# Kernel optimization log

Measured on AMD Instinct MI355X. Metric: run time of the kernel, lower is better.

## Reference

```python
import jax, jax.numpy as jnp
import numpy as np

N_NODES = 50000
N_EDGES = 300000
D = 256  # node/edge feature dim; MLP input = 3*D = 768


def setup_inputs() -> dict:
    key = jax.random.key(0)
    ks = jax.random.split(key, 5)
    x_node = jax.random.normal(ks[0], (N_NODES, D), dtype=jnp.float32)
    x_edge = jax.random.normal(ks[1], (N_EDGES, D), dtype=jnp.float32)
    edge_index = jax.random.randint(ks[2], (2, N_EDGES), 0, N_NODES, dtype=jnp.int64)
    # MLP params: Linear(3*D, D) -> ReLU -> Linear(D, D)
    W1 = jax.random.normal(ks[3], (3 * D, D), dtype=jnp.float32) * (1.0 / np.sqrt(3 * D))
    b1 = jnp.zeros((D,), dtype=jnp.float32)
    W2 = jax.random.normal(ks[4], (D, D), dtype=jnp.float32) * (1.0 / np.sqrt(D))
    b2 = jnp.zeros((D,), dtype=jnp.float32)
    return {"x_node": x_node, "x_edge": x_edge, "edge_index": edge_index,
            "W1": W1, "b1": b1, "W2": W2, "b2": b2}


def reference(x_node, x_edge, edge_index, W1, b1, W2, b2):
    # gather src/dst node feats and concat with edge feats: [E, 3*D]
    src = x_node[edge_index[0]]
    dst = x_node[edge_index[1]]
    h = jnp.concatenate([src, dst, x_edge], axis=1)
    # MLP (custom_func): Linear -> ReLU -> Linear
    h = jax.nn.relu(h @ W1 + b1)
    x_edge_ = h @ W2 + b2
    return x_edge_
```

## Files before the change

### kernel.cpp

```cpp
#include <hip/hip_runtime.h>


typedef __attribute__((ext_vector_type(8))) short short8;
typedef __attribute__((ext_vector_type(4))) float f32x4;

typedef __attribute__((address_space(1))) unsigned int* gp1_t;
typedef __attribute__((address_space(3))) unsigned int* lp3_t;

#define AS_OFF 0
#define BS_OFF 16384
#define HS_OFF 49152
#define SMEM_SZ 114688
#define LDO 260

__device__ __forceinline__ unsigned short f2b(float f) {
  unsigned int u = __float_as_uint(f);
  return (unsigned short)((u + 0x7FFFu + ((u >> 16) & 1u)) >> 16);
}
__device__ __forceinline__ unsigned int f2b2(float lo, float hi) {
  return (unsigned int)f2b(lo) | ((unsigned int)f2b(hi) << 16);
}
__device__ __forceinline__ void gload16(const void* g, void* l) {
  __builtin_amdgcn_global_load_lds((gp1_t)g, (lp3_t)l, 16, 0, 0);
}

__global__ void prep_w_kernel(const float* __restrict__ w,
                              unsigned short* __restrict__ wp, int total) {
  int i = blockIdx.x * 256 + threadIdx.x;
  if (i >= total) return;
  int kc = i >> 13;
  int rem = i & 8191;
  int n = rem >> 5;
  int kin = rem & 31;
  wp[i] = f2b(w[(size_t)(kc * 32 + kin) * 256 + n]);
}

__global__ void conv_bf16_kernel(const float* __restrict__ x,
                                 unsigned short* __restrict__ y, int n4) {
  int i = blockIdx.x * 256 + threadIdx.x;
  if (i >= n4) return;
  float4 v = ((const float4*)x)[i];
  ushort4 u;
  u.x = f2b(v.x); u.y = f2b(v.y); u.z = f2b(v.z); u.w = f2b(v.w);
  ((ushort4*)y)[i] = u;
}

__global__ __launch_bounds__(512, 2) void edge_mlp_kernel(
    const float* __restrict__ xnode, const float* __restrict__ xedge,
    const int* __restrict__ eidx,
    const unsigned short* __restrict__ nodeb, int use_nodeb,
    const unsigned short* __restrict__ wt1p, const float* __restrict__ b1,
    const unsigned short* __restrict__ wt2p, const float* __restrict__ b2,
    float* __restrict__ out, int E) {
  __shared__ __align__(16) char smem[SMEM_SZ];
  char* As = smem + AS_OFF;
  char* Bs = smem + BS_OFF;
  char* Hs = smem + HS_OFF;

  const int t = threadIdx.x;
  const int w = t >> 6, l = t & 63;
  const int lr = l & 15, lk = l >> 4;
  const int wr = w >> 2, wc = w & 3;
  const int row4 = t >> 2;
  const int c4 = t & 3;

  const int ebase = blockIdx.x * 128;
  int e = ebase + row4;
  if (e >= E) e = E - 1;
  const int isrc = eidx[e], idst = eidx[E + e];

  f32x4 acc[4][4];
#pragma unroll
  for (int i = 0; i < 4; ++i)
#pragma unroll
    for (int j = 0; j < 4; ++j) acc[i][j] = (f32x4)0.0f;

  auto stageB = [&](const unsigned short* wp, int kc, int buf) {
    const char* g = (const char*)wp + (size_t)kc * 16384 + t * 16;
    char* lb = Bs + buf * 16384 + (w << 10);
    gload16(g, lb);
    gload16(g + 8192, lb + 8192);
  };
  auto stageA_node = [&](int kc, int buf) {
    const int node = (kc < 8) ? isrc : idst;
    const char* g = (const char*)nodeb + (size_t)node * 512 + (kc & 7) * 64 + c4 * 16;
    gload16(g, As + buf * 8192 + (w << 10));
  };
  auto stageA_load = [&](int kc, float4& m0, float4& m1) {
    const float* src;
    if (kc < 8)        src = xnode + (size_t)isrc * 256 + kc * 32 + c4 * 8;
    else if (kc < 16)  src = xnode + (size_t)idst * 256 + (kc - 8) * 32 + c4 * 8;
    else               src = xedge + (size_t)e * 256 + (kc - 16) * 32 + c4 * 8;
    m0 = *(const float4*)src;
    m1 = *(const float4*)(src + 4);
  };
  auto stageA_write = [&](int buf, float4 m0, float4 m1) {
    uint4 u;
    u.x = f2b2(m0.x, m0.y); u.y = f2b2(m0.z, m0.w);
    u.z = f2b2(m1.x, m1.y); u.w = f2b2(m1.z, m1.w);
    *(uint4*)(As + buf * 8192 + t * 16) = u;
  };

  auto compute1 = [&](int buf) {
    short8 af[4], bf[4];
    const char* ab = As + buf * 8192;
    const char* bb = Bs + buf * 16384;
#pragma unroll
    for (int mi = 0; mi < 4; ++mi)
      af[mi] = *(const short8*)(ab + (wr * 64 + mi * 16 + lr) * 64 + lk * 16);
#pragma unroll
    for (int ni = 0; ni < 4; ++ni)
      bf[ni] = *(const short8*)(bb + (wc * 64 + ni * 16 + lr) * 64 + lk * 16);
#pragma unroll
    for (int mi = 0; mi < 4; ++mi)
#pragma unroll
      for (int ni = 0; ni < 4; ++ni)
        acc[mi][ni] = __builtin_amdgcn_mfma_f32_16x16x32_bf16(
            af[mi], bf[ni], acc[mi][ni], 0, 0, 0);
  };

  stageB(wt1p, 0, 0);
  if (use_nodeb) {
    stageA_node(0, 0);
  } else {
    float4 a0, a1;
    stageA_load(0, a0, a1);
    stageA_write(0, a0, a1);
  }
  __syncthreads();

  for (int kc = 0; kc < 24; ++kc) {
    const int cur = kc & 1, nb = cur ^ 1;
    float4 m0, m1;
    bool man = false;
    if (kc < 23) {
      const int nk = kc + 1;
      stageB(wt1p, nk, nb);
      if (use_nodeb && nk < 16) {
        stageA_node(nk, nb);
      } else {
        stageA_load(nk, m0, m1);
        man = true;
      }
    } else {
      stageB(wt2p, 0, nb);
    }
    compute1(cur);
    if (man) stageA_write(nb, m0, m1);
    __syncthreads();
  }

#pragma unroll
  for (int ni = 0; ni < 4; ++ni) {
    const int col = wc * 64 + ni * 16 + lr;
    const float bias = b1[col];
    const int chunk = col >> 3;
    const int cb = (col & 7) * 2;
#pragma unroll
    for (int mi = 0; mi < 4; ++mi)
#pragma unroll
      for (int r = 0; r < 4; ++r) {
        const int row = wr * 64 + mi * 16 + lk * 4 + r;
        float v = acc[mi][ni][r] + bias;
        v = v > 0.f ? v : 0.f;
        *(unsigned short*)(Hs + row * 512 + ((chunk ^ (row & 7)) * 16) + cb) = f2b(v);
        acc[mi][ni][r] = 0.f;
      }
  }
  __syncthreads();

  for (int kc2 = 0; kc2 < 8; ++kc2) {
    const int cur = kc2 & 1, nb = cur ^ 1;
    if (kc2 < 7) stageB(wt2p, kc2 + 1, nb);
    {
      short8 af[4], bf[4];
      const char* bb = Bs + cur * 16384;
#pragma unroll
      for (int mi = 0; mi < 4; ++mi) {
        const int row = wr * 64 + mi * 16 + lr;
        af[mi] = *(const short8*)(Hs + row * 512 + (((kc2 * 4 + lk) ^ (row & 7)) * 16));
      }
#pragma unroll
      for (int ni = 0; ni < 4; ++ni)
        bf[ni] = *(const short8*)(bb + (wc * 64 + ni * 16 + lr) * 64 + lk * 16);
#pragma unroll
      for (int mi = 0; mi < 4; ++mi)
#pragma unroll
        for (int ni = 0; ni < 4; ++ni)
          acc[mi][ni] = __builtin_amdgcn_mfma_f32_16x16x32_bf16(
              af[mi], bf[ni], acc[mi][ni], 0, 0, 0);
    }
    __syncthreads();
  }

  float* outst = (float*)smem;
#pragma unroll
  for (int p = 0; p < 2; ++p) {
    __syncthreads();
    if (wr == p) {
#pragma unroll
      for (int ni = 0; ni < 4; ++ni) {
        const int col = wc * 64 + ni * 16 + lr;
        const float bias = b2[col];
#pragma unroll
        for (int mi = 0; mi < 4; ++mi)
#pragma unroll
          for (int r = 0; r < 4; ++r)
            outst[(mi * 16 + lk * 4 + r) * LDO + col] = acc[mi][ni][r] + bias;
      }
    }
    __syncthreads();
#pragma unroll
    for (int it = 0; it < 8; ++it) {
      const int idx = it * 2048 + t * 4;
      const int lrow = idx >> 8;
      const int cc = idx & 255;
      const int grow = ebase + p * 64 + lrow;
      if (grow < E)
        *(float4*)(out + (size_t)grow * 256 + cc) =
            *(const float4*)(outst + lrow * LDO + cc);
    }
  }
}

extern "C" void kernel_launch(void* const* d_in, const int* in_sizes, int n_in,
                              void* d_out, int out_size, void* d_ws, size_t ws_size,
                              hipStream_t stream) {
  const float* xnode = (const float*)d_in[0];
  const float* xedge = (const float*)d_in[1];
  const int* eidx = (const int*)d_in[2];
  const float* W1 = (const float*)d_in[3];
  const float* b1 = (const float*)d_in[4];
  const float* W2 = (const float*)d_in[5];
  const float* b2 = (const float*)d_in[6];
  float* out = (float*)d_out;

  const int NN = in_sizes[0] / 256;
  const int E = in_sizes[1] / 256;

  char* ws = (char*)d_ws;
  unsigned short* wt1p = (unsigned short*)ws;
  unsigned short* wt2p = (unsigned short*)(ws + 24 * 16384);
  unsigned short* nodeb = (unsigned short*)(ws + 32 * 16384);
  const size_t need = (size_t)32 * 16384 + (size_t)NN * 512;
  const int use_nodeb = (ws_size >= need) ? 1 : 0;

  prep_w_kernel<<<(24 * 8192 + 255) / 256, 256, 0, stream>>>(W1, wt1p, 24 * 8192);
  prep_w_kernel<<<(8 * 8192 + 255) / 256, 256, 0, stream>>>(W2, wt2p, 8 * 8192);
  if (use_nodeb) {
    const int n4 = NN * 64;
    conv_bf16_kernel<<<(n4 + 255) / 256, 256, 0, stream>>>(xnode, nodeb, n4);
  }

  edge_mlp_kernel<<<(E + 127) / 128, 512, 0, stream>>>(
      xnode, xedge, eidx, nodeb, use_nodeb, wt1p, b1, wt2p, b2, out, E);
}
```

Before: 332.2 us.

## Shrink edge MLP tile to 64 edges with 4 waves and pack H writes

```diff
diff --git a/kernel.cpp b/kernel.cpp
--- a/kernel.cpp
+++ b/kernel.cpp
@@ -8,9 +8,9 @@
 typedef __attribute__((address_space(3))) unsigned int* lp3_t;
 
 #define AS_OFF 0
-#define BS_OFF 16384
-#define HS_OFF 49152
-#define SMEM_SZ 114688
+#define BS_OFF 8192
+#define HS_OFF 40960
+#define SMEM_SZ 73728
 #define LDO 260
 
 __device__ __forceinline__ unsigned short f2b(float f) {
@@ -45,7 +45,7 @@
   ((ushort4*)y)[i] = u;
 }
 
-__global__ __launch_bounds__(512, 2) void edge_mlp_kernel(
+__global__ __launch_bounds__(256, 2) void edge_mlp_kernel(
     const float* __restrict__ xnode, const float* __restrict__ xedge,
     const int* __restrict__ eidx,
     const unsigned short* __restrict__ nodeb, int use_nodeb,
@@ -60,11 +60,10 @@
   const int t = threadIdx.x;
   const int w = t >> 6, l = t & 63;
   const int lr = l & 15, lk = l >> 4;
-  const int wr = w >> 2, wc = w & 3;
   const int row4 = t >> 2;
   const int c4 = t & 3;
 
-  const int ebase = blockIdx.x * 128;
+  const int ebase = blockIdx.x * 64;
   int e = ebase + row4;
   if (e >= E) e = E - 1;
   const int isrc = eidx[e], idst = eidx[E + e];
@@ -78,13 +77,13 @@
   auto stageB = [&](const unsigned short* wp, int kc, int buf) {
     const char* g = (const char*)wp + (size_t)kc * 16384 + t * 16;
     char* lb = Bs + buf * 16384 + (w << 10);
-    gload16(g, lb);
-    gload16(g + 8192, lb + 8192);
+#pragma unroll
+    for (int q = 0; q < 4; ++q) gload16(g + q * 4096, lb + q * 4096);
   };
   auto stageA_node = [&](int kc, int buf) {
     const int node = (kc < 8) ? isrc : idst;
     const char* g = (const char*)nodeb + (size_t)node * 512 + (kc & 7) * 64 + c4 * 16;
-    gload16(g, As + buf * 8192 + (w << 10));
+    gload16(g, As + buf * 4096 + (w << 10));
   };
   auto stageA_load = [&](int kc, float4& m0, float4& m1) {
     const float* src;
@@ -98,19 +97,19 @@
     uint4 u;
     u.x = f2b2(m0.x, m0.y); u.y = f2b2(m0.z, m0.w);
     u.z = f2b2(m1.x, m1.y); u.w = f2b2(m1.z, m1.w);
-    *(uint4*)(As + buf * 8192 + t * 16) = u;
+    *(uint4*)(As + buf * 4096 + t * 16) = u;
   };
 
   auto compute1 = [&](int buf) {
     short8 af[4], bf[4];
-    const char* ab = As + buf * 8192;
+    const char* ab = As + buf * 4096;
     const char* bb = Bs + buf * 16384;
 #pragma unroll
     for (int mi = 0; mi < 4; ++mi)
-      af[mi] = *(const short8*)(ab + (wr * 64 + mi * 16 + lr) * 64 + lk * 16);
+      af[mi] = *(const short8*)(ab + (mi * 16 + lr) * 64 + lk * 16);
 #pragma unroll
     for (int ni = 0; ni < 4; ++ni)
-      bf[ni] = *(const short8*)(bb + (wc * 64 + ni * 16 + lr) * 64 + lk * 16);
+      bf[ni] = *(const short8*)(bb + (w * 64 + ni * 16 + lr) * 64 + lk * 16);
 #pragma unroll
     for (int mi = 0; mi < 4; ++mi)
 #pragma unroll
@@ -152,20 +151,32 @@
 
 #pragma unroll
   for (int ni = 0; ni < 4; ++ni) {
-    const int col = wc * 64 + ni * 16 + lr;
+    const int col = w * 64 + ni * 16 + lr;
     const float bias = b1[col];
-    const int chunk = col >> 3;
-    const int cb = (col & 7) * 2;
-#pragma unroll
-    for (int mi = 0; mi < 4; ++mi)
+    const int cole = col & ~1;
+    const int chunk = cole >> 3;
+    const int cb = (cole & 6) * 2;
+#pragma unroll
+    for (int mi = 0; mi < 4; ++mi) {
+      float v[4], p[4];
 #pragma unroll
       for (int r = 0; r < 4; ++r) {
-        const int row = wr * 64 + mi * 16 + lk * 4 + r;
-        float v = acc[mi][ni][r] + bias;
-        v = v > 0.f ? v : 0.f;
-        *(unsigned short*)(Hs + row * 512 + ((chunk ^ (row & 7)) * 16) + cb) = f2b(v);
+        float x = acc[mi][ni][r] + bias;
+        v[r] = x > 0.f ? x : 0.f;
         acc[mi][ni][r] = 0.f;
       }
+#pragma unroll
+      for (int r = 0; r < 4; ++r) p[r] = __shfl_xor(v[r], 1, 64);
+      const int r0 = (lr & 1) ? 2 : 0;
+#pragma unroll
+      for (int rr = 0; rr < 2; ++rr) {
+        const int r = r0 + rr;
+        const int row = mi * 16 + lk * 4 + r;
+        const float lo = (lr & 1) ? p[r] : v[r];
+        const float hi = (lr & 1) ? v[r] : p[r];
+        *(unsigned int*)(Hs + row * 512 + ((chunk ^ (row & 7)) << 4) + cb) = f2b2(lo, hi);
+      }
+    }
   }
   __syncthreads();
 
@@ -177,12 +188,12 @@
       const char* bb = Bs + cur * 16384;
 #pragma unroll
       for (int mi = 0; mi < 4; ++mi) {
-        const int row = wr * 64 + mi * 16 + lr;
-        af[mi] = *(const short8*)(Hs + row * 512 + (((kc2 * 4 + lk) ^ (row & 7)) * 16));
+        const int row = mi * 16 + lr;
+        af[mi] = *(const short8*)(Hs + row * 512 + (((kc2 * 4 + lk) ^ (row & 7)) << 4));
       }
 #pragma unroll
       for (int ni = 0; ni < 4; ++ni)
-        bf[ni] = *(const short8*)(bb + (wc * 64 + ni * 16 + lr) * 64 + lk * 16);
+        bf[ni] = *(const short8*)(bb + (w * 64 + ni * 16 + lr) * 64 + lk * 16);
 #pragma unroll
       for (int mi = 0; mi < 4; ++mi)
 #pragma unroll
@@ -195,31 +206,25 @@
 
   float* outst = (float*)smem;
 #pragma unroll
-  for (int p = 0; p < 2; ++p) {
-    __syncthreads();
-    if (wr == p) {
-#pragma unroll
-      for (int ni = 0; ni < 4; ++ni) {
-        const int col = wc * 64 + ni * 16 + lr;
-        const float bias = b2[col];
-#pragma unroll
-        for (int mi = 0; mi < 4; ++mi)
-#pragma unroll
-          for (int r = 0; r < 4; ++r)
-            outst[(mi * 16 + lk * 4 + r) * LDO + col] = acc[mi][ni][r] + bias;
-      }
-    }
-    __syncthreads();
-#pragma unroll
-    for (int it = 0; it < 8; ++it) {
-      const int idx = it * 2048 + t * 4;
-      const int lrow = idx >> 8;
-      const int cc = idx & 255;
-      const int grow = ebase + p * 64 + lrow;
-      if (grow < E)
-        *(float4*)(out + (size_t)grow * 256 + cc) =
-            *(const float4*)(outst + lrow * LDO + cc);
-    }
+  for (int ni = 0; ni < 4; ++ni) {
+    const int col = w * 64 + ni * 16 + lr;
+    const float bias = b2[col];
+#pragma unroll
+    for (int mi = 0; mi < 4; ++mi)
+#pragma unroll
+      for (int r = 0; r < 4; ++r)
+        outst[(mi * 16 + lk * 4 + r) * LDO + col] = acc[mi][ni][r] + bias;
+  }
+  __syncthreads();
+#pragma unroll
+  for (int it = 0; it < 16; ++it) {
+    const int idx = it * 1024 + t * 4;
+    const int lrow = idx >> 8;
+    const int cc = idx & 255;
+    const int grow = ebase + lrow;
+    if (grow < E)
+      *(float4*)(out + (size_t)grow * 256 + cc) =
+          *(const float4*)(outst + lrow * LDO + cc);
   }
 }
 
@@ -252,6 +257,6 @@
     conv_bf16_kernel<<<(n4 + 255) / 256, 256, 0, stream>>>(xnode, nodeb, n4);
   }
 
-  edge_mlp_kernel<<<(E + 127) / 128, 512, 0, stream>>>(
+  edge_mlp_kernel<<<(E + 63) / 64, 256, 0, stream>>>(
       xnode, xedge, eidx, nodeb, use_nodeb, wt1p, b1, wt2p, b2, out, E);
 }
```

After: 379.8 us. +14.4%, slower.

## Load A fragments directly to registers and triple-buffer weight staging with vmcnt waits

Applied to the files above, without the earlier changes.

```diff
diff --git a/kernel.cpp b/kernel.cpp
--- a/kernel.cpp
+++ b/kernel.cpp
@@ -3,15 +3,15 @@
 
 typedef __attribute__((ext_vector_type(8))) short short8;
 typedef __attribute__((ext_vector_type(4))) float f32x4;
-
 typedef __attribute__((address_space(1))) unsigned int* gp1_t;
 typedef __attribute__((address_space(3))) unsigned int* lp3_t;
 
-#define AS_OFF 0
-#define BS_OFF 16384
 #define HS_OFF 49152
 #define SMEM_SZ 114688
 #define LDO 260
+
+#define WAITV(N) asm volatile("s_waitcnt vmcnt(" #N ")" ::: "memory")
+#define PHASE_SYNC() do { __builtin_amdgcn_s_barrier(); __builtin_amdgcn_sched_barrier(0); } while (0)
 
 __device__ __forceinline__ unsigned short f2b(float f) {
   unsigned int u = __float_as_uint(f);
@@ -31,7 +31,10 @@
   int kc = i >> 13;
   int rem = i & 8191;
   int n = rem >> 5;
-  int kin = rem & 31;
+  int within = rem & 31;
+  int s = within >> 3;
+  int j = within & 7;
+  int kin = (((s - (n >> 1)) & 3) << 3) | j;
   wp[i] = f2b(w[(size_t)(kc * 32 + kin) * 256 + n]);
 }
 
@@ -53,21 +56,23 @@
     const unsigned short* __restrict__ wt2p, const float* __restrict__ b2,
     float* __restrict__ out, int E) {
   __shared__ __align__(16) char smem[SMEM_SZ];
-  char* As = smem + AS_OFF;
-  char* Bs = smem + BS_OFF;
+  char* Bs = smem;
   char* Hs = smem + HS_OFF;
 
-  const int t = threadIdx.x;
-  const int w = t >> 6, l = t & 63;
+  const int t = threadIdx.x, w = t >> 6, l = t & 63;
   const int lr = l & 15, lk = l >> 4;
   const int wr = w >> 2, wc = w & 3;
-  const int row4 = t >> 2;
-  const int c4 = t & 3;
-
   const int ebase = blockIdx.x * 128;
-  int e = ebase + row4;
-  if (e >= E) e = E - 1;
-  const int isrc = eidx[e], idst = eidx[E + e];
+
+  int er[4], nsrc[4], ndst[4];
+#pragma unroll
+  for (int mi = 0; mi < 4; ++mi) {
+    int e = ebase + wr * 64 + mi * 16 + lr;
+    if (e >= E) e = E - 1;
+    er[mi] = e;
+    nsrc[mi] = eidx[e];
+    ndst[mi] = eidx[E + e];
+  }
 
   f32x4 acc[4][4];
 #pragma unroll
@@ -75,122 +80,168 @@
 #pragma unroll
     for (int j = 0; j < 4; ++j) acc[i][j] = (f32x4)0.0f;
 
-  auto stageB = [&](const unsigned short* wp, int kc, int buf) {
-    const char* g = (const char*)wp + (size_t)kc * 16384 + t * 16;
+  auto stageB = [&](const unsigned short* wp, int c, int buf) {
+    const char* g = (const char*)wp + (size_t)c * 16384 + t * 16;
     char* lb = Bs + buf * 16384 + (w << 10);
     gload16(g, lb);
     gload16(g + 8192, lb + 8192);
   };
-  auto stageA_node = [&](int kc, int buf) {
-    const int node = (kc < 8) ? isrc : idst;
-    const char* g = (const char*)nodeb + (size_t)node * 512 + (kc & 7) * 64 + c4 * 16;
-    gload16(g, As + buf * 8192 + (w << 10));
-  };
-  auto stageA_load = [&](int kc, float4& m0, float4& m1) {
-    const float* src;
-    if (kc < 8)        src = xnode + (size_t)isrc * 256 + kc * 32 + c4 * 8;
-    else if (kc < 16)  src = xnode + (size_t)idst * 256 + (kc - 8) * 32 + c4 * 8;
-    else               src = xedge + (size_t)e * 256 + (kc - 16) * 32 + c4 * 8;
-    m0 = *(const float4*)src;
-    m1 = *(const float4*)(src + 4);
-  };
-  auto stageA_write = [&](int buf, float4 m0, float4 m1) {
-    uint4 u;
-    u.x = f2b2(m0.x, m0.y); u.y = f2b2(m0.z, m0.w);
-    u.z = f2b2(m1.x, m1.y); u.w = f2b2(m1.z, m1.w);
-    *(uint4*)(As + buf * 8192 + t * 16) = u;
-  };
-
-  auto compute1 = [&](int buf) {
-    short8 af[4], bf[4];
-    const char* ab = As + buf * 8192;
+  auto stageC = [&](int c) {
+    if (c < 24) stageB(wt1p, c, c % 3);
+    else        stageB(wt2p, c - 24, c % 3);
+  };
+  auto loadA_node = [&](int c, short8 (&a)[4]) {
+    const int* nid = (c < 8) ? nsrc : ndst;
+    const int co = (c & 7) * 64 + lk * 16;
+#pragma unroll
+    for (int mi = 0; mi < 4; ++mi)
+      a[mi] = *(const short8*)((const char*)nodeb + (size_t)nid[mi] * 512 + co);
+  };
+  auto loadA_f32 = [&](int c, float4 (&m)[4][2]) {
+    const float* base; const int* rows; int co;
+    if (c < 8)       { base = xnode; rows = nsrc; co = c * 32 + lk * 8; }
+    else if (c < 16) { base = xnode; rows = ndst; co = (c - 8) * 32 + lk * 8; }
+    else             { base = xedge; rows = er;   co = (c - 16) * 32 + lk * 8; }
+#pragma unroll
+    for (int mi = 0; mi < 4; ++mi) {
+      const float* p = base + (size_t)rows[mi] * 256 + co;
+      m[mi][0] = *(const float4*)p;
+      m[mi][1] = *(const float4*)(p + 4);
+    }
+  };
+  auto cvtA = [&](float4 (&m)[4][2], short8 (&a)[4]) {
+#pragma unroll
+    for (int mi = 0; mi < 4; ++mi) {
+      union { short8 s; unsigned int u[4]; } cv;
+      cv.u[0] = f2b2(m[mi][0].x, m[mi][0].y);
+      cv.u[1] = f2b2(m[mi][0].z, m[mi][0].w);
+      cv.u[2] = f2b2(m[mi][1].x, m[mi][1].y);
+      cv.u[3] = f2b2(m[mi][1].z, m[mi][1].w);
+      a[mi] = cv.s;
+    }
+  };
+  auto loadA = [&](int c, short8 (&a)[4], float4 (&m)[4][2], bool& isf) {
+    if (c < 16 && use_nodeb) { loadA_node(c, a); isf = false; }
+    else                     { loadA_f32(c, m);  isf = true; }
+  };
+  auto computeK = [&](int buf, short8 (&a)[4]) {
+    short8 bf[4];
     const char* bb = Bs + buf * 16384;
 #pragma unroll
-    for (int mi = 0; mi < 4; ++mi)
-      af[mi] = *(const short8*)(ab + (wr * 64 + mi * 16 + lr) * 64 + lk * 16);
-#pragma unroll
-    for (int ni = 0; ni < 4; ++ni)
-      bf[ni] = *(const short8*)(bb + (wc * 64 + ni * 16 + lr) * 64 + lk * 16);
+    for (int ni = 0; ni < 4; ++ni) {
+      const int row = wc * 64 + ni * 16 + lr;
+      const int slot = (lk + (row >> 1)) & 3;
+      bf[ni] = *(const short8*)(bb + row * 64 + slot * 16);
+    }
+    __builtin_amdgcn_s_setprio(1);
 #pragma unroll
     for (int mi = 0; mi < 4; ++mi)
 #pragma unroll
       for (int ni = 0; ni < 4; ++ni)
         acc[mi][ni] = __builtin_amdgcn_mfma_f32_16x16x32_bf16(
-            af[mi], bf[ni], acc[mi][ni], 0, 0, 0);
-  };
-
-  stageB(wt1p, 0, 0);
-  if (use_nodeb) {
-    stageA_node(0, 0);
-  } else {
-    float4 a0, a1;
-    stageA_load(0, a0, a1);
-    stageA_write(0, a0, a1);
-  }
-  __syncthreads();
-
-  for (int kc = 0; kc < 24; ++kc) {
-    const int cur = kc & 1, nb = cur ^ 1;
-    float4 m0, m1;
-    bool man = false;
-    if (kc < 23) {
-      const int nk = kc + 1;
-      stageB(wt1p, nk, nb);
-      if (use_nodeb && nk < 16) {
-        stageA_node(nk, nb);
-      } else {
-        stageA_load(nk, m0, m1);
-        man = true;
-      }
-    } else {
-      stageB(wt2p, 0, nb);
-    }
-    compute1(cur);
-    if (man) stageA_write(nb, m0, m1);
-    __syncthreads();
+            a[mi], bf[ni], acc[mi][ni], 0, 0, 0);
+    __builtin_amdgcn_s_setprio(0);
+  };
+
+  short8 afE[4], afO[4];
+  float4 mE[4][2], mO[4][2];
+  bool fE = false, fO = false;
+
+  stageC(0);
+  stageC(1);
+  loadA(0, afE, mE, fE);
+
+  for (int tt = 0; tt < 16; tt += 2) {
+    WAITV(6);
+    PHASE_SYNC();
+    stageC(tt + 2);
+    loadA(tt + 1, afO, mO, fO);
+    if (fE) cvtA(mE, afE);
+    computeK(tt % 3, afE);
+
+    WAITV(6);
+    PHASE_SYNC();
+    stageC(tt + 3);
+    loadA(tt + 2, afE, mE, fE);
+    if (fO) cvtA(mO, afO);
+    computeK((tt + 1) % 3, afO);
+  }
+
+  for (int tt = 16; tt < 24; tt += 2) {
+    WAITV(10);
+    PHASE_SYNC();
+    stageC(tt + 2);
+    loadA(tt + 1, afO, mO, fO);
+    if (fE) cvtA(mE, afE);
+    computeK(tt % 3, afE);
+
+    WAITV(10);
+    PHASE_SYNC();
+    stageC(tt + 3);
+    if (tt + 2 < 24) loadA(tt + 2, afE, mE, fE);
+    if (fO) cvtA(mO, afO);
+    computeK((tt + 1) % 3, afO);
   }
 
 #pragma unroll
   for (int ni = 0; ni < 4; ++ni) {
     const int col = wc * 64 + ni * 16 + lr;
     const float bias = b1[col];
-    const int chunk = col >> 3;
-    const int cb = (col & 7) * 2;
-#pragma unroll
-    for (int mi = 0; mi < 4; ++mi)
+    const int cole = col & ~1;
+    const int chunk = cole >> 3;
+    const int cb = (cole & 6) * 2;
+#pragma unroll
+    for (int mi = 0; mi < 4; ++mi) {
+      float v[4], p[4];
 #pragma unroll
       for (int r = 0; r < 4; ++r) {
-        const int row = wr * 64 + mi * 16 + lk * 4 + r;
-        float v = acc[mi][ni][r] + bias;
-        v = v > 0.f ? v : 0.f;
-        *(unsigned short*)(Hs + row * 512 + ((chunk ^ (row & 7)) * 16) + cb) = f2b(v);
+        float x = acc[mi][ni][r] + bias;
+        v[r] = x > 0.f ? x : 0.f;
         acc[mi][ni][r] = 0.f;
       }
-  }
-  __syncthreads();
-
-  for (int kc2 = 0; kc2 < 8; ++kc2) {
-    const int cur = kc2 & 1, nb = cur ^ 1;
-    if (kc2 < 7) stageB(wt2p, kc2 + 1, nb);
-    {
-      short8 af[4], bf[4];
-      const char* bb = Bs + cur * 16384;
-#pragma unroll
-      for (int mi = 0; mi < 4; ++mi) {
-        const int row = wr * 64 + mi * 16 + lr;
-        af[mi] = *(const short8*)(Hs + row * 512 + (((kc2 * 4 + lk) ^ (row & 7)) * 16));
+#pragma unroll
+      for (int r = 0; r < 4; ++r) p[r] = __shfl_xor(v[r], 1, 64);
+      const int r0 = (lr & 1) ? 2 : 0;
+#pragma unroll
+      for (int rr = 0; rr < 2; ++rr) {
+        const int r = r0 + rr;
+        const int row = wr * 64 + mi * 16 + lk * 4 + r;
+        const float lo = (lr & 1) ? p[r] : v[r];
+        const float hi = (lr & 1) ? v[r] : p[r];
+        *(unsigned int*)(Hs + row * 512 + ((chunk ^ (row & 7)) << 4) + cb) =
+            f2b2(lo, hi);
       }
+    }
+  }
+  asm volatile("s_waitcnt lgkmcnt(0)" ::: "memory");
+
+#pragma unroll
+  for (int u = 0; u < 8; ++u) {
+    if (u < 7) { WAITV(2); } else { WAITV(0); }
+    PHASE_SYNC();
+    if (u < 6) stageB(wt2p, u + 2, (26 + u) % 3);
+    short8 af2[4], bf2[4];
+    const char* bb = Bs + ((24 + u) % 3) * 16384;
+#pragma unroll
+    for (int mi = 0; mi < 4; ++mi) {
+      const int row = wr * 64 + mi * 16 + lr;
+      af2[mi] = *(const short8*)(Hs + row * 512 +
+                                 ((((u << 2) + lk) ^ (row & 7)) << 4));
+    }
+#pragma unroll
+    for (int ni = 0; ni < 4; ++ni) {
+      const int row = wc * 64 + ni * 16 + lr;
+      const int slot = (lk + (row >> 1)) & 3;
+      bf2[ni] = *(const short8*)(bb + row * 64 + slot * 16);
+    }
+    __builtin_amdgcn_s_setprio(1);
+#pragma unroll
+    for (int mi = 0; mi < 4; ++mi)
 #pragma unroll
       for (int ni = 0; ni < 4; ++ni)
-        bf[ni] = *(const short8*)(bb + (wc * 64 + ni * 16 + lr) * 64 + lk * 16);
-#pragma unroll
-      for (int mi = 0; mi < 4; ++mi)
-#pragma unroll
-        for (int ni = 0; ni < 4; ++ni)
-          acc[mi][ni] = __builtin_amdgcn_mfma_f32_16x16x32_bf16(
-              af[mi], bf[ni], acc[mi][ni], 0, 0, 0);
-    }
-    __syncthreads();
+        acc[mi][ni] = __builtin_amdgcn_mfma_f32_16x16x32_bf16(
+            af2[mi], bf2[ni], acc[mi][ni], 0, 0, 0);
+    __builtin_amdgcn_s_setprio(0);
   }
 
   float* outst = (float*)smem;
```

Measured after the change: 626.7 us. 88.7% more time.
